# Performance work log

Hardware: AMD Instinct MI355X
Metric: run time of the kernel (lower is better)

Reference implementation:

```python
import jax, jax.numpy as jnp
import numpy as np

B, V, L, H, E, META = 2048, 4096, 10, 512, 256, 15
TAU = 1.2
SOS = 0
EOS = 0


def setup_inputs() -> dict:
    key = jax.random.key(0)
    ks = jax.random.split(key, 8)
    hidden_state = jax.random.normal(ks[0], (B, META), jnp.float32)
    W_in = jax.random.normal(ks[1], (META, H), jnp.float32) * 0.1
    b_in = jnp.zeros((H,), jnp.float32)
    embedding = jax.random.normal(ks[2], (V, E), jnp.float32) * 0.1
    W_ih = jax.random.normal(ks[3], (4 * H, E), jnp.float32) * (1.0 / np.sqrt(E))
    W_hh = jax.random.normal(ks[4], (4 * H, H), jnp.float32) * (1.0 / np.sqrt(H))
    b_ih = jnp.zeros((4 * H,), jnp.float32)
    # forget-gate bias initialized to 1 (reset_parameters)
    b_hh = jnp.zeros((4 * H,), jnp.float32).at[H:2 * H].set(1.0)
    W_out = jax.random.normal(ks[5], (H, V), jnp.float32) * 0.02
    b_out = jnp.zeros((V,), jnp.float32)
    u = jax.random.uniform(ks[6], (L, B, V), jnp.float32, 1e-8, 1.0 - 1e-8)
    gumbel = -jnp.log(-jnp.log(u))
    return {"hidden_state": hidden_state, "W_in": W_in, "b_in": b_in,
            "embedding": embedding, "W_ih": W_ih, "W_hh": W_hh,
            "b_ih": b_ih, "b_hh": b_hh, "W_out": W_out, "b_out": b_out,
            "gumbel": gumbel}


def reference(hidden_state, W_in, b_in, embedding, W_ih, W_hh, b_ih, b_hh,
              W_out, b_out, gumbel):
    initial_length = L + 1
    h0 = hidden_state @ W_in + b_in              # [B,H] input_module (meta)
    c0 = jnp.zeros_like(h0)
    tok0 = jnp.zeros((B, V), jnp.float32).at[:, SOS].set(1.0)  # one-hot sos
    sl0 = jnp.full((B,), initial_length, jnp.int32)

    def step(carry, xs):
        h, c, tok, sl = carry
        i, g = xs
        emb = tok @ embedding                                  # [B,E]
        gates = emb @ W_ih.T + b_ih + h @ W_hh.T + b_hh        # [B,4H]
        ig, fg, gg, og = jnp.split(gates, 4, axis=1)
        c = jax.nn.sigmoid(fg) * c + jax.nn.sigmoid(ig) * jnp.tanh(gg)
        h = jax.nn.sigmoid(og) * jnp.tanh(c)
        logits = h @ W_out + b_out                             # [B,V]
        logp = jax.nn.log_softmax(logits, axis=1)
        p = jnp.exp(logp)
        ent = -jnp.sum(p * logp, axis=1)                       # Categorical entropy
        # gumbel_softmax(p, tau, hard=True): softmax((log p + g)/tau), straight-through
        y = jax.nn.softmax((logp + g) / TAU, axis=1)
        hard = jax.nn.one_hot(jnp.argmax(y, axis=1), V, dtype=y.dtype)
        tok_new = jax.lax.stop_gradient(hard - y) + y
        mask = (hard[:, EOS] == 1.0) & (sl == initial_length)
        sl = jnp.where(mask, i + 2, sl)  # seq_pos = i+1, set to seq_pos+1
        return (h, c, tok_new, sl), (tok_new, emb, ent)

    (_, _, _, seq_lengths), (toks, embeds, ents) = jax.lax.scan(
        step, (h0, c0, tok0, sl0), (jnp.arange(L, dtype=jnp.int32), gumbel))
    output = jnp.concatenate([tok0[:, None, :], jnp.transpose(toks, (1, 0, 2))], axis=1)  # [B,L+1,V]
    embeds_out = jnp.transpose(embeds, (1, 0, 2))              # [B,L,E]
    entropy = jnp.mean(jnp.sum(ents, axis=0)) / L
    sentence_probability = jnp.zeros((B, V), jnp.float32)      # only filled in eval mode
    return output, seq_lengths, entropy, embeds_out, sentence_probability
```

## Files before the change

kernel.cpp:

```cpp
#include <hip/hip_runtime.h>
#include <hip/hip_bf16.h>
#include <math.h>

typedef unsigned short u16;
typedef __attribute__((ext_vector_type(8))) short bf16x8;
typedef __attribute__((ext_vector_type(4))) float f32x4;

#define B_    2048
#define V_    4096
#define L_    10
#define H_    512
#define E_    256
#define META_ 15
#define H4_   2048
#define W6_   (H4_ + V_)
#define EOS_  0
#define INIT_LEN_ (L_ + 1)

constexpr size_t OUT_SL  = (size_t)B_ * (L_ + 1) * V_;
constexpr size_t OUT_ENT = OUT_SL + B_;
constexpr size_t OUT_EMB = OUT_ENT + 1;
constexpr size_t OUT_SP  = OUT_EMB + (size_t)B_ * L_ * E_;

constexpr size_t WS_E2G     = 0;
constexpr size_t WS_LOGITS  = WS_E2G    + (size_t)V_ * H4_;
constexpr size_t WS_G       = WS_LOGITS + (size_t)B_ * V_;
constexpr size_t WS_C       = WS_G      + (size_t)B_ * H4_;
constexpr size_t WS_F32_END = WS_C      + (size_t)B_ * H_;
constexpr size_t U_W6_HI    = 0;
constexpr size_t U_W6_LO    = U_W6_HI + (size_t)W6_ * H_;
constexpr size_t U_HHI      = U_W6_LO + (size_t)W6_ * H_;
constexpr size_t U_HLO      = U_HHI   + (size_t)B_ * H_;
constexpr size_t U_END      = U_HLO   + (size_t)B_ * H_;

__device__ __forceinline__ u16 f2bf(float f) {
    union { __hip_bfloat16 b; u16 u; } cv; cv.b = __float2bfloat16(f); return cv.u;
}
__device__ __forceinline__ float bf2f(u16 u) {
    union { u16 u; __hip_bfloat16 b; } cv; cv.u = u; return __bfloat162float(cv.b);
}

__device__ __forceinline__ void gld16(const u16* g, void* l) {
    __builtin_amdgcn_global_load_lds(
        (const __attribute__((address_space(1))) unsigned int*)g,
        (__attribute__((address_space(3))) unsigned int*)l, 16, 0, 0);
}

template <int EPI>
__global__ __launch_bounds__(256)
void gemm3(const u16* __restrict__ Ah, const u16* __restrict__ Al,
           const u16* __restrict__ Bh, const u16* __restrict__ Bl,
           float* __restrict__ C0, float* __restrict__ C1, int K,
           const float* __restrict__ bias0, const float* __restrict__ bias1,
           int xoff)
{
    __shared__ u16 As[2][128][32];
    __shared__ u16 Bs[2][128][32];
    const int tid  = threadIdx.x;
    const int lane = tid & 63;
    const int wave = tid >> 6;
    const int wm = wave >> 1, wn = wave & 1;

    const int nwg  = gridDim.x * gridDim.y;
    const int bid  = blockIdx.y * gridDim.x + blockIdx.x;
    const int w    = (bid & 7) * (nwg >> 3) + (bid >> 3);
    const int colb = w / gridDim.y + xoff;
    const int rowb = w % gridDim.y;
    const int col0 = colb * 128;
    const int row0 = rowb * 128;

    const int srow = tid >> 2;
    const int scol = (tid & 3) * 8;
    const size_t aoff = (size_t)(row0 + srow) * K + scol;
    const size_t boff = (size_t)(col0 + srow) * K + scol;
    const size_t skip = (size_t)64 * K;

    u16* lA0 = &As[0][0][0];
    u16* lA1 = &As[1][0][0];
    u16* lB0 = &Bs[0][0][0];
    u16* lB1 = &Bs[1][0][0];
    const int d0 = tid * 8;
    const int d1 = d0 + 2048;

    f32x4 acc[4][4] = {};
    const int fr = lane & 15;
    const int kq = lane >> 4;

    for (int k0 = 0; k0 < K; k0 += 32) {
        __syncthreads();
        gld16(Ah + aoff + k0,        lA0 + d0);
        gld16(Ah + aoff + k0 + skip, lA0 + d1);
        gld16(Al + aoff + k0,        lA1 + d0);
        gld16(Al + aoff + k0 + skip, lA1 + d1);
        gld16(Bh + boff + k0,        lB0 + d0);
        gld16(Bh + boff + k0 + skip, lB0 + d1);
        gld16(Bl + boff + k0,        lB1 + d0);
        gld16(Bl + boff + k0 + skip, lB1 + d1);
        __syncthreads();

        bf16x8 ah[4], al[4], bh[4], bl[4];
#pragma unroll
        for (int i = 0; i < 4; ++i) {
            ah[i] = *(const bf16x8*)&As[0][wm * 64 + i * 16 + fr][kq * 8];
            al[i] = *(const bf16x8*)&As[1][wm * 64 + i * 16 + fr][kq * 8];
            bh[i] = *(const bf16x8*)&Bs[0][wn * 64 + i * 16 + fr][kq * 8];
            bl[i] = *(const bf16x8*)&Bs[1][wn * 64 + i * 16 + fr][kq * 8];
        }
#pragma unroll
        for (int mi = 0; mi < 4; ++mi)
#pragma unroll
            for (int ni = 0; ni < 4; ++ni) {
                acc[mi][ni] = __builtin_amdgcn_mfma_f32_16x16x32_bf16(ah[mi], bh[ni], acc[mi][ni], 0, 0, 0);
                acc[mi][ni] = __builtin_amdgcn_mfma_f32_16x16x32_bf16(ah[mi], bl[ni], acc[mi][ni], 0, 0, 0);
                acc[mi][ni] = __builtin_amdgcn_mfma_f32_16x16x32_bf16(al[mi], bh[ni], acc[mi][ni], 0, 0, 0);
            }
    }

    const int cc0 = col0 + wn * 64 + fr;
    float* Cbase;
    int ldc, ccol;
    bool addBias;
    if (EPI == 0) {
        Cbase = C0; ldc = H4_; ccol = cc0; addBias = true;
    } else {
        const bool isG = (col0 < H4_);
        Cbase = isG ? C0 : C1;
        ldc   = isG ? H4_ : V_;
        ccol  = isG ? cc0 : cc0 - H4_;
        addBias = !isG;
    }
#pragma unroll
    for (int mi = 0; mi < 4; ++mi) {
#pragma unroll
        for (int r = 0; r < 4; ++r) {
            const int grow = row0 + wm * 64 + mi * 16 + kq * 4 + r;
            float* cp = Cbase + (size_t)grow * ldc + ccol;
#pragma unroll
            for (int ni = 0; ni < 4; ++ni) {
                float v = acc[mi][ni][r];
                if (EPI == 0) v += bias0[ccol + ni * 16] + bias1[ccol + ni * 16];
                if (EPI == 1 && addBias) v += bias0[ccol + ni * 16];
                cp[ni * 16] = v;
            }
        }
    }
}

template <bool LAST>
__global__ __launch_bounds__(256)
void step_merge(const float* __restrict__ logits, const float* __restrict__ gumbel,
                const float* __restrict__ G, const float* __restrict__ e2g,
                const float* __restrict__ embedding,
                u16* __restrict__ h_hi, u16* __restrict__ h_lo,
                float* __restrict__ c, float* __restrict__ out,
                int* __restrict__ sl, float* __restrict__ ents, int step)
{
    const int b   = blockIdx.x;
    const int tid = threadIdx.x;
    const float* lrow = logits + (size_t)b * V_;
    const float* grow = gumbel + ((size_t)step * B_ + b) * V_;
    __shared__ float lsm[V_];
    __shared__ float red_m[4], red_bv[4], red_s[4], red_t[4];
    __shared__ int   red_bi[4];
    __shared__ float s_M;
    __shared__ int   s_bi;

    float m = -3.4e38f, bv = -3.4e38f;
    int bi = 0x7fffffff;
    for (int q = tid; q < V_ / 4; q += 256) {
        float4 l4 = ((const float4*)lrow)[q];
        float4 g4 = ((const float4*)grow)[q];
        ((float4*)lsm)[q] = l4;
        m = fmaxf(m, fmaxf(fmaxf(l4.x, l4.y), fmaxf(l4.z, l4.w)));
        float p; const int i4 = q * 4;
        p = l4.x + g4.x; if (p > bv) { bv = p; bi = i4; }
        p = l4.y + g4.y; if (p > bv) { bv = p; bi = i4 + 1; }
        p = l4.z + g4.z; if (p > bv) { bv = p; bi = i4 + 2; }
        p = l4.w + g4.w; if (p > bv) { bv = p; bi = i4 + 3; }
    }
#pragma unroll
    for (int off = 32; off > 0; off >>= 1) {
        m = fmaxf(m, __shfl_down(m, off));
        float obv = __shfl_down(bv, off);
        int   obi = __shfl_down(bi, off);
        if (obv > bv || (obv == bv && obi < bi)) { bv = obv; bi = obi; }
    }
    const int wave = tid >> 6, lane = tid & 63;
    if (lane == 0) { red_m[wave] = m; red_bv[wave] = bv; red_bi[wave] = bi; }
    __syncthreads();
    if (tid == 0) {
        m = red_m[0]; bv = red_bv[0]; bi = red_bi[0];
        for (int w = 1; w < 4; ++w) {
            m = fmaxf(m, red_m[w]);
            if (red_bv[w] > bv || (red_bv[w] == bv && red_bi[w] < bi)) {
                bv = red_bv[w]; bi = red_bi[w];
            }
        }
        s_M = m; s_bi = bi;
    }
    __syncthreads();
    const float M = s_M;
    const int amax = s_bi;

    float s = 0.f, t = 0.f;
    for (int q = tid; q < V_; q += 256) {
        const float l = lsm[q];
        const float e = __expf(l - M);
        s += e; t += e * l;
    }
#pragma unroll
    for (int off = 32; off > 0; off >>= 1) {
        s += __shfl_down(s, off);
        t += __shfl_down(t, off);
    }
    if (lane == 0) { red_s[wave] = s; red_t[wave] = t; }

    float* orow = out + ((size_t)b * (L_ + 1) + step + 1) * V_;
    const float4 z4 = make_float4(0.f, 0.f, 0.f, 0.f);
    for (int q = tid; q < V_ / 4; q += 256) ((float4*)orow)[q] = z4;
    __syncthreads();
    if (tid == 0) {
        const float ss = red_s[0] + red_s[1] + red_s[2] + red_s[3];
        const float tt = red_t[0] + red_t[1] + red_t[2] + red_t[3];
        ents[b] += (M + logf(ss)) - tt / ss;
        orow[amax] = 1.0f;
        if (amax == EOS_ && sl[b] == INIT_LEN_) sl[b] = step + 2;
    }

    if (!LAST) {
        const float* Gr = G + (size_t)b * H4_;
        const float* er = e2g + (size_t)amax * H4_;
#pragma unroll
        for (int jj = 0; jj < 2; ++jj) {
            const int j = tid + jj * 256;
            const float ig = Gr[j]          + er[j];
            const float fg = Gr[H_ + j]     + er[H_ + j];
            const float gg = Gr[2 * H_ + j] + er[2 * H_ + j];
            const float og = Gr[3 * H_ + j] + er[3 * H_ + j];
            const float si = 1.f / (1.f + expf(-ig));
            const float sf = 1.f / (1.f + expf(-fg));
            const float so = 1.f / (1.f + expf(-og));
            const size_t idx = (size_t)b * H_ + j;
            const float cn = sf * c[idx] + si * tanhf(gg);
            c[idx] = cn;
            const float hv = so * tanhf(cn);
            const u16 hh = f2bf(hv);
            h_hi[idx] = hh;
            h_lo[idx] = f2bf(hv - bf2f(hh));
        }
        if (tid < E_)
            out[OUT_EMB + ((size_t)b * L_ + step + 1) * E_ + tid] =
                embedding[(size_t)amax * E_ + tid];
    }
}

__global__ __launch_bounds__(256)
void split_wout(const float* __restrict__ W_out, u16* __restrict__ hiT,
                u16* __restrict__ loT)
{
    __shared__ float t[32][33];
    const int v0 = blockIdx.x * 32, k0 = blockIdx.y * 32;
    const int x = threadIdx.x & 31, y = threadIdx.x >> 5;
    for (int yy = y; yy < 32; yy += 8)
        t[yy][x] = W_out[(size_t)(k0 + yy) * V_ + v0 + x];
    __syncthreads();
    for (int yy = y; yy < 32; yy += 8) {
        const float v = t[x][yy];
        const u16 h = f2bf(v);
        hiT[(size_t)(v0 + yy) * H_ + k0 + x] = h;
        loT[(size_t)(v0 + yy) * H_ + k0 + x] = f2bf(v - bf2f(h));
    }
}

__global__ __launch_bounds__(256)
void split_mat(const float* __restrict__ X, u16* __restrict__ hi,
               u16* __restrict__ lo)
{
    const int i = blockIdx.x * 256 + threadIdx.x;
    float4 v = ((const float4*)X)[i];
    const u16 h0 = f2bf(v.x), h1 = f2bf(v.y), h2 = f2bf(v.z), h3 = f2bf(v.w);
    ((ushort4*)hi)[i] = make_ushort4(h0, h1, h2, h3);
    ((ushort4*)lo)[i] = make_ushort4(f2bf(v.x - bf2f(h0)), f2bf(v.y - bf2f(h1)),
                                     f2bf(v.z - bf2f(h2)), f2bf(v.w - bf2f(h3)));
}

__global__ __launch_bounds__(256)
void h0_kernel(const float* __restrict__ hs, const float* __restrict__ W_in,
               const float* __restrict__ b_in, u16* __restrict__ h_hi,
               u16* __restrict__ h_lo, float* __restrict__ c)
{
    const int idx = blockIdx.x * 256 + threadIdx.x;
    const int b = idx >> 9, j = idx & 511;
    float acc = b_in[j];
#pragma unroll
    for (int e = 0; e < META_; ++e)
        acc = fmaf(hs[b * META_ + e], W_in[e * H_ + j], acc);
    const u16 hh = f2bf(acc);
    h_hi[idx] = hh;
    h_lo[idx] = f2bf(acc - bf2f(hh));
    c[idx] = 0.f;
}

__global__ __launch_bounds__(256)
void init_outputs(float* __restrict__ out, int* __restrict__ tok,
                  int* __restrict__ sl, float* __restrict__ ents)
{
    const int tid = blockIdx.x * 256 + threadIdx.x;
    {
        const int b = tid >> 10;
        const int q = tid & 1023;
        float4 z = make_float4(0.f, 0.f, 0.f, 0.f);
        if (q == 0) z.x = 1.0f;
        ((float4*)out)[(size_t)b * ((L_ + 1) * V_ / 4) + q] = z;
    }
    for (size_t t = tid; t < (size_t)B_ * V_; t += (size_t)gridDim.x * 256)
        out[OUT_SP + t] = 0.f;
    if (tid < B_) { tok[tid] = 0; sl[tid] = INIT_LEN_; ents[tid] = 0.f; }
}

__global__ __launch_bounds__(256)
void lstm_cell(const float* __restrict__ G, const float* __restrict__ e2g,
               u16* __restrict__ h_hi, u16* __restrict__ h_lo,
               float* __restrict__ c, const float* __restrict__ embedding,
               const int* __restrict__ tok, float* __restrict__ out, int step)
{
    const int idx = blockIdx.x * 256 + threadIdx.x;
    const int b = idx >> 9, j = idx & 511;
    const size_t g0 = (size_t)b * H4_;
    const size_t e0 = (size_t)tok[b] * H4_;
    const float ig = G[g0 + j]          + e2g[e0 + j];
    const float fg = G[g0 + H_ + j]     + e2g[e0 + H_ + j];
    const float gg = G[g0 + 2 * H_ + j] + e2g[e0 + 2 * H_ + j];
    const float og = G[g0 + 3 * H_ + j] + e2g[e0 + 3 * H_ + j];
    const float si = 1.f / (1.f + expf(-ig));
    const float sf = 1.f / (1.f + expf(-fg));
    const float so = 1.f / (1.f + expf(-og));
    const float cn = sf * c[idx] + si * tanhf(gg);
    c[idx] = cn;
    const float hv = so * tanhf(cn);
    const u16 hh = f2bf(hv);
    h_hi[idx] = hh;
    h_lo[idx] = f2bf(hv - bf2f(hh));
    if (j < E_)
        out[OUT_EMB + ((size_t)b * L_ + step) * E_ + j] =
            embedding[(size_t)tok[b] * E_ + j];
}

__global__ __launch_bounds__(256)
void finalize(const int* __restrict__ sl, const float* __restrict__ ents,
              float* __restrict__ out)
{
    const int tid = threadIdx.x;
    float s = 0.f;
    for (int b = tid; b < B_; b += 256) {
        s += ents[b];
        out[OUT_SL + b] = (float)sl[b];
    }
    __shared__ float red[4];
#pragma unroll
    for (int off = 32; off > 0; off >>= 1) s += __shfl_down(s, off);
    if ((tid & 63) == 0) red[tid >> 6] = s;
    __syncthreads();
    if (tid == 0)
        out[OUT_ENT] = (red[0] + red[1] + red[2] + red[3]) / (float)B_ / (float)L_;
}

extern "C" void kernel_launch(void* const* d_in, const int* in_sizes, int n_in,
                              void* d_out, int out_size, void* d_ws, size_t ws_size,
                              hipStream_t stream)
{
    const float* hidden    = (const float*)d_in[0];
    const float* W_in      = (const float*)d_in[1];
    const float* b_in      = (const float*)d_in[2];
    const float* embedding = (const float*)d_in[3];
    const float* W_ih      = (const float*)d_in[4];
    const float* W_hh      = (const float*)d_in[5];
    const float* b_ih      = (const float*)d_in[6];
    const float* b_hh      = (const float*)d_in[7];
    const float* W_out     = (const float*)d_in[8];
    const float* b_out     = (const float*)d_in[9];
    const float* gumbel    = (const float*)d_in[10];
    float* out = (float*)d_out;

    float* ws    = (float*)d_ws;
    float* E2G   = ws + WS_E2G;
    float* logit = ws + WS_LOGITS;
    float* G     = ws + WS_G;
    float* c     = ws + WS_C;
    u16*   wsu   = (u16*)(ws + WS_F32_END);
    u16* w6_hi   = wsu + U_W6_HI;
    u16* w6_lo   = wsu + U_W6_LO;
    u16* h_hi    = wsu + U_HHI;
    u16* h_lo    = wsu + U_HLO;
    int* tok     = (int*)(wsu + U_END);
    int* sl      = tok + B_;
    float* ents  = (float*)(sl + B_);
    u16* emb_hi  = (u16*)logit;
    u16* emb_lo  = emb_hi + (size_t)V_ * E_;
    u16* wih_hi  = emb_lo + (size_t)V_ * E_;
    u16* wih_lo  = wih_hi + (size_t)H4_ * E_;

    split_mat<<<(H4_ * H_ / 4) / 256, 256, 0, stream>>>(W_hh, w6_hi, w6_lo);
    split_wout<<<dim3(V_ / 32, H_ / 32), 256, 0, stream>>>(
        W_out, w6_hi + (size_t)H4_ * H_, w6_lo + (size_t)H4_ * H_);
    split_mat<<<(V_ * E_ / 4) / 256, 256, 0, stream>>>(embedding, emb_hi, emb_lo);
    split_mat<<<(H4_ * E_ / 4) / 256, 256, 0, stream>>>(W_ih, wih_hi, wih_lo);
    h0_kernel<<<(B_ * H_) / 256, 256, 0, stream>>>(hidden, W_in, b_in, h_hi, h_lo, c);
    init_outputs<<<(B_ * V_ / 4) / 256, 256, 0, stream>>>(out, tok, sl, ents);
    gemm3<0><<<dim3(H4_ / 128, V_ / 128), 256, 0, stream>>>(
        emb_hi, emb_lo, wih_hi, wih_lo, E2G, nullptr, E_, b_ih, b_hh, 0);
    gemm3<1><<<dim3(H4_ / 128, B_ / 128), 256, 0, stream>>>(
        h_hi, h_lo, w6_hi, w6_lo, G, logit, H_, b_out, nullptr, 0);
    lstm_cell<<<(B_ * H_) / 256, 256, 0, stream>>>(G, E2G, h_hi, h_lo, c,
                                                   embedding, tok, out, 0);

    for (int i = 0; i < L_; ++i) {
        if (i < L_ - 1) {
            gemm3<1><<<dim3(W6_ / 128, B_ / 128), 256, 0, stream>>>(
                h_hi, h_lo, w6_hi, w6_lo, G, logit, H_, b_out, nullptr, 0);
            step_merge<false><<<B_, 256, 0, stream>>>(
                logit, gumbel, G, E2G, embedding, h_hi, h_lo, c, out,
                sl, ents, i);
        } else {
            gemm3<1><<<dim3(V_ / 128, B_ / 128), 256, 0, stream>>>(
                h_hi, h_lo, w6_hi, w6_lo, G, logit, H_, b_out, nullptr,
                H4_ / 128);
            step_merge<true><<<B_, 256, 0, stream>>>(
                logit, gumbel, G, E2G, embedding, h_hi, h_lo, c, out,
                sl, ents, i);
        }
    }
    finalize<<<1, 256, 0, stream>>>(sl, ents, out);
}
```

Baseline: 835.2 us.

## Pre-pack GEMM operands into tiled layout and use 32x32x16 MFMA

The recurrent h and the combined W_hh/W_out weights are now stored in a tile-packed layout (128-row blocks, k-chunks of 32, 8-element groups), so each GEMM stage is a contiguous 8 KB block loaded straight to LDS. The main per-step GEMM is rewritten to use 32x32x16 bf16 MFMA with 2x2 accumulators per wave instead of 16x16x32, which cuts LDS reads per MFMA. The h writers and weight repack kernels scatter into the packed layout, trading coalesced stores for faster GEMM loads. The packed LDS layout may also bring bank conflicts.

```diff
diff --git a/kernel.cpp b/kernel.cpp
--- a/kernel.cpp
+++ b/kernel.cpp
@@ -5,6 +5,7 @@
 typedef unsigned short u16;
 typedef __attribute__((ext_vector_type(8))) short bf16x8;
 typedef __attribute__((ext_vector_type(4))) float f32x4;
+typedef __attribute__((ext_vector_type(16))) float f32x16;
 
 #define B_    2048
 #define V_    4096
@@ -27,11 +28,11 @@
 constexpr size_t WS_G       = WS_LOGITS + (size_t)B_ * V_;
 constexpr size_t WS_C       = WS_G      + (size_t)B_ * H4_;
 constexpr size_t WS_F32_END = WS_C      + (size_t)B_ * H_;
-constexpr size_t U_W6_HI    = 0;
-constexpr size_t U_W6_LO    = U_W6_HI + (size_t)W6_ * H_;
-constexpr size_t U_HHI      = U_W6_LO + (size_t)W6_ * H_;
-constexpr size_t U_HLO      = U_HHI   + (size_t)B_ * H_;
-constexpr size_t U_END      = U_HLO   + (size_t)B_ * H_;
+constexpr size_t U_BH       = 0;
+constexpr size_t U_BL       = U_BH + (size_t)W6_ * H_;
+constexpr size_t U_AH       = U_BL + (size_t)W6_ * H_;
+constexpr size_t U_AL       = U_AH + (size_t)B_ * H_;
+constexpr size_t U_END      = U_AL + (size_t)B_ * H_;
 
 __device__ __forceinline__ u16 f2bf(float f) {
     union { __hip_bfloat16 b; u16 u; } cv; cv.b = __float2bfloat16(f); return cv.u;
@@ -39,20 +40,113 @@
 __device__ __forceinline__ float bf2f(u16 u) {
     union { u16 u; __hip_bfloat16 b; } cv; cv.u = u; return __bfloat162float(cv.b);
 }
-
 __device__ __forceinline__ void gld16(const u16* g, void* l) {
     __builtin_amdgcn_global_load_lds(
         (const __attribute__((address_space(1))) unsigned int*)g,
         (__attribute__((address_space(3))) unsigned int*)l, 16, 0, 0);
 }
 
-template <int EPI>
-__global__ __launch_bounds__(256)
-void gemm3(const u16* __restrict__ Ah, const u16* __restrict__ Al,
-           const u16* __restrict__ Bh, const u16* __restrict__ Bl,
-           float* __restrict__ C0, float* __restrict__ C1, int K,
-           const float* __restrict__ bias0, const float* __restrict__ bias1,
-           int xoff)
+__device__ __forceinline__ size_t a_pk(int r, int k) {
+    return (size_t)(r >> 7) * 65536 + (size_t)(k >> 5) * 4096 +
+           (size_t)((k >> 3) & 3) * 1024 + (size_t)(r & 127) * 8 + (k & 7);
+}
+
+__global__ __launch_bounds__(256)
+void gemm32(const u16* __restrict__ Ah, const u16* __restrict__ Al,
+            const u16* __restrict__ Bh, const u16* __restrict__ Bl,
+            float* __restrict__ C0, float* __restrict__ C1,
+            const float* __restrict__ bias0, int xoff)
+{
+    __shared__ u16 As[2][4096];
+    __shared__ u16 Bs[2][4096];
+    const int tid  = threadIdx.x;
+    const int lane = tid & 63;
+    const int wave = tid >> 6;
+    const int wm = wave >> 1, wn = wave & 1;
+    const int l31 = lane & 31, lh = lane >> 5;
+
+    const int nwg  = gridDim.x * gridDim.y;
+    const int bid  = blockIdx.y * gridDim.x + blockIdx.x;
+    const int w    = (bid & 7) * (nwg >> 3) + (bid >> 3);
+    const int colb = w / gridDim.y + xoff;
+    const int rowb = w % gridDim.y;
+    const int col0 = colb * 128;
+    const int row0 = rowb * 128;
+
+    const u16* Ah_p = Ah + (size_t)rowb * 65536;
+    const u16* Al_p = Al + (size_t)rowb * 65536;
+    const u16* Bh_p = Bh + (size_t)colb * 65536;
+    const u16* Bl_p = Bl + (size_t)colb * 65536;
+    const int d0 = tid * 8;
+    const int d1 = d0 + 2048;
+
+    const int abase = lh * 1024 + (wm * 64 + l31) * 8;
+    const int bbase = lh * 1024 + (wn * 64 + l31) * 8;
+
+    f32x16 acc[2][2] = {};
+
+    for (int t = 0; t < 16; ++t) {
+        const int g0 = t * 4096;
+        __syncthreads();
+        gld16(Ah_p + g0 + d0, &As[0][d0]);
+        gld16(Ah_p + g0 + d1, &As[0][d1]);
+        gld16(Al_p + g0 + d0, &As[1][d0]);
+        gld16(Al_p + g0 + d1, &As[1][d1]);
+        gld16(Bh_p + g0 + d0, &Bs[0][d0]);
+        gld16(Bh_p + g0 + d1, &Bs[0][d1]);
+        gld16(Bl_p + g0 + d0, &Bs[1][d0]);
+        gld16(Bl_p + g0 + d1, &Bs[1][d1]);
+        __syncthreads();
+
+        bf16x8 ah[2][2], al[2][2], bh[2][2], bl[2][2];
+#pragma unroll
+        for (int kh = 0; kh < 2; ++kh)
+#pragma unroll
+            for (int g = 0; g < 2; ++g) {
+                ah[kh][g] = *(const bf16x8*)&As[0][abase + kh * 2048 + g * 256];
+                al[kh][g] = *(const bf16x8*)&As[1][abase + kh * 2048 + g * 256];
+                bh[kh][g] = *(const bf16x8*)&Bs[0][bbase + kh * 2048 + g * 256];
+                bl[kh][g] = *(const bf16x8*)&Bs[1][bbase + kh * 2048 + g * 256];
+            }
+#pragma unroll
+        for (int kh = 0; kh < 2; ++kh)
+#pragma unroll
+            for (int rg = 0; rg < 2; ++rg)
+#pragma unroll
+                for (int cg = 0; cg < 2; ++cg) {
+                    acc[rg][cg] = __builtin_amdgcn_mfma_f32_32x32x16_bf16(
+                        ah[kh][rg], bh[kh][cg], acc[rg][cg], 0, 0, 0);
+                    acc[rg][cg] = __builtin_amdgcn_mfma_f32_32x32x16_bf16(
+                        ah[kh][rg], bl[kh][cg], acc[rg][cg], 0, 0, 0);
+                    acc[rg][cg] = __builtin_amdgcn_mfma_f32_32x32x16_bf16(
+                        al[kh][rg], bh[kh][cg], acc[rg][cg], 0, 0, 0);
+                }
+    }
+
+    const bool isG  = (col0 < H4_);
+    float* Cb       = isG ? C0 : C1;
+    const int ldc   = isG ? H4_ : V_;
+    const int ccol0 = (isG ? col0 : col0 - H4_) + wn * 64 + l31;
+    const int rbase = row0 + wm * 64 + 4 * lh;
+#pragma unroll
+    for (int rg = 0; rg < 2; ++rg)
+#pragma unroll
+        for (int cg = 0; cg < 2; ++cg) {
+            const int ccol = ccol0 + cg * 32;
+            const float bv = isG ? 0.f : bias0[ccol];
+#pragma unroll
+            for (int reg = 0; reg < 16; ++reg) {
+                const int row = rbase + rg * 32 + (reg & 3) + 8 * (reg >> 2);
+                Cb[(size_t)row * ldc + ccol] = acc[rg][cg][reg] + bv;
+            }
+        }
+}
+
+__global__ __launch_bounds__(256)
+void gemm_e2g(const u16* __restrict__ Ah, const u16* __restrict__ Al,
+              const u16* __restrict__ Bh, const u16* __restrict__ Bl,
+              float* __restrict__ C0, int K,
+              const float* __restrict__ bias0, const float* __restrict__ bias1)
 {
     __shared__ u16 As[2][128][32];
     __shared__ u16 Bs[2][128][32];
@@ -60,11 +154,10 @@
     const int lane = tid & 63;
     const int wave = tid >> 6;
     const int wm = wave >> 1, wn = wave & 1;
-
     const int nwg  = gridDim.x * gridDim.y;
     const int bid  = blockIdx.y * gridDim.x + blockIdx.x;
     const int w    = (bid & 7) * (nwg >> 3) + (bid >> 3);
-    const int colb = w / gridDim.y + xoff;
+    const int colb = w / gridDim.y;
     const int rowb = w % gridDim.y;
     const int col0 = colb * 128;
     const int row0 = rowb * 128;
@@ -117,31 +210,15 @@
     }
 
     const int cc0 = col0 + wn * 64 + fr;
-    float* Cbase;
-    int ldc, ccol;
-    bool addBias;
-    if (EPI == 0) {
-        Cbase = C0; ldc = H4_; ccol = cc0; addBias = true;
-    } else {
-        const bool isG = (col0 < H4_);
-        Cbase = isG ? C0 : C1;
-        ldc   = isG ? H4_ : V_;
-        ccol  = isG ? cc0 : cc0 - H4_;
-        addBias = !isG;
-    }
 #pragma unroll
     for (int mi = 0; mi < 4; ++mi) {
 #pragma unroll
         for (int r = 0; r < 4; ++r) {
             const int grow = row0 + wm * 64 + mi * 16 + kq * 4 + r;
-            float* cp = Cbase + (size_t)grow * ldc + ccol;
-#pragma unroll
-            for (int ni = 0; ni < 4; ++ni) {
-                float v = acc[mi][ni][r];
-                if (EPI == 0) v += bias0[ccol + ni * 16] + bias1[ccol + ni * 16];
-                if (EPI == 1 && addBias) v += bias0[ccol + ni * 16];
-                cp[ni * 16] = v;
-            }
+            float* cp = C0 + (size_t)grow * H4_ + cc0;
+#pragma unroll
+            for (int ni = 0; ni < 4; ++ni)
+                cp[ni * 16] = acc[mi][ni][r] + bias0[cc0 + ni * 16] + bias1[cc0 + ni * 16];
         }
     }
 }
@@ -245,8 +322,9 @@
             c[idx] = cn;
             const float hv = so * tanhf(cn);
             const u16 hh = f2bf(hv);
-            h_hi[idx] = hh;
-            h_lo[idx] = f2bf(hv - bf2f(hh));
+            const size_t p = a_pk(b, j);
+            h_hi[p] = hh;
+            h_lo[p] = f2bf(hv - bf2f(hh));
         }
         if (tid < E_)
             out[OUT_EMB + ((size_t)b * L_ + step + 1) * E_ + tid] =
@@ -255,8 +333,23 @@
 }
 
 __global__ __launch_bounds__(256)
-void split_wout(const float* __restrict__ W_out, u16* __restrict__ hiT,
-                u16* __restrict__ loT)
+void repack_whh(const float* __restrict__ W_hh, u16* __restrict__ Bh,
+                u16* __restrict__ Bl)
+{
+    const int i = blockIdx.x * 256 + threadIdx.x;
+    float4 v = ((const float4*)W_hh)[i];
+    const int col = (i * 4) >> 9;
+    const int k   = (i * 4) & 511;
+    const size_t p = a_pk(col, k);
+    const u16 h0 = f2bf(v.x), h1 = f2bf(v.y), h2 = f2bf(v.z), h3 = f2bf(v.w);
+    *(ushort4*)(Bh + p) = make_ushort4(h0, h1, h2, h3);
+    *(ushort4*)(Bl + p) = make_ushort4(f2bf(v.x - bf2f(h0)), f2bf(v.y - bf2f(h1)),
+                                       f2bf(v.z - bf2f(h2)), f2bf(v.w - bf2f(h3)));
+}
+
+__global__ __launch_bounds__(256)
+void repack_wout(const float* __restrict__ W_out, u16* __restrict__ Bh,
+                 u16* __restrict__ Bl)
 {
     __shared__ float t[32][33];
     const int v0 = blockIdx.x * 32, k0 = blockIdx.y * 32;
@@ -266,9 +359,10 @@
     __syncthreads();
     for (int yy = y; yy < 32; yy += 8) {
         const float v = t[x][yy];
+        const size_t p = a_pk(2048 + v0 + yy, k0 + x);
         const u16 h = f2bf(v);
-        hiT[(size_t)(v0 + yy) * H_ + k0 + x] = h;
-        loT[(size_t)(v0 + yy) * H_ + k0 + x] = f2bf(v - bf2f(h));
+        Bh[p] = h;
+        Bl[p] = f2bf(v - bf2f(h));
     }
 }
 
@@ -286,8 +380,8 @@
 
 __global__ __launch_bounds__(256)
 void h0_kernel(const float* __restrict__ hs, const float* __restrict__ W_in,
-               const float* __restrict__ b_in, u16* __restrict__ h_hi,
-               u16* __restrict__ h_lo, float* __restrict__ c)
+               const float* __restrict__ b_in, u16* __restrict__ Ah,
+               u16* __restrict__ Al, float* __restrict__ c)
 {
     const int idx = blockIdx.x * 256 + threadIdx.x;
     const int b = idx >> 9, j = idx & 511;
@@ -296,8 +390,9 @@
     for (int e = 0; e < META_; ++e)
         acc = fmaf(hs[b * META_ + e], W_in[e * H_ + j], acc);
     const u16 hh = f2bf(acc);
-    h_hi[idx] = hh;
-    h_lo[idx] = f2bf(acc - bf2f(hh));
+    const size_t p = a_pk(b, j);
+    Ah[p] = hh;
+    Al[p] = f2bf(acc - bf2f(hh));
     c[idx] = 0.f;
 }
 
@@ -320,7 +415,7 @@
 
 __global__ __launch_bounds__(256)
 void lstm_cell(const float* __restrict__ G, const float* __restrict__ e2g,
-               u16* __restrict__ h_hi, u16* __restrict__ h_lo,
+               u16* __restrict__ Ah, u16* __restrict__ Al,
                float* __restrict__ c, const float* __restrict__ embedding,
                const int* __restrict__ tok, float* __restrict__ out, int step)
 {
@@ -339,8 +434,9 @@
     c[idx] = cn;
     const float hv = so * tanhf(cn);
     const u16 hh = f2bf(hv);
-    h_hi[idx] = hh;
-    h_lo[idx] = f2bf(hv - bf2f(hh));
+    const size_t p = a_pk(b, j);
+    Ah[p] = hh;
+    Al[p] = f2bf(hv - bf2f(hh));
     if (j < E_)
         out[OUT_EMB + ((size_t)b * L_ + step) * E_ + j] =
             embedding[(size_t)tok[b] * E_ + j];
@@ -388,10 +484,10 @@
     float* G     = ws + WS_G;
     float* c     = ws + WS_C;
     u16*   wsu   = (u16*)(ws + WS_F32_END);
-    u16* w6_hi   = wsu + U_W6_HI;
-    u16* w6_lo   = wsu + U_W6_LO;
-    u16* h_hi    = wsu + U_HHI;
-    u16* h_lo    = wsu + U_HLO;
+    u16* Bh_pk   = wsu + U_BH;
+    u16* Bl_pk   = wsu + U_BL;
+    u16* Ah_pk   = wsu + U_AH;
+    u16* Al_pk   = wsu + U_AL;
     int* tok     = (int*)(wsu + U_END);
     int* sl      = tok + B_;
     float* ents  = (float*)(sl + B_);
@@ -400,33 +496,32 @@
     u16* wih_hi  = emb_lo + (size_t)V_ * E_;
     u16* wih_lo  = wih_hi + (size_t)H4_ * E_;
 
-    split_mat<<<(H4_ * H_ / 4) / 256, 256, 0, stream>>>(W_hh, w6_hi, w6_lo);
-    split_wout<<<dim3(V_ / 32, H_ / 32), 256, 0, stream>>>(
-        W_out, w6_hi + (size_t)H4_ * H_, w6_lo + (size_t)H4_ * H_);
+    repack_whh<<<(H4_ * H_ / 4) / 256, 256, 0, stream>>>(W_hh, Bh_pk, Bl_pk);
+    repack_wout<<<dim3(V_ / 32, H_ / 32), 256, 0, stream>>>(W_out, Bh_pk, Bl_pk);
     split_mat<<<(V_ * E_ / 4) / 256, 256, 0, stream>>>(embedding, emb_hi, emb_lo);
     split_mat<<<(H4_ * E_ / 4) / 256, 256, 0, stream>>>(W_ih, wih_hi, wih_lo);
-    h0_kernel<<<(B_ * H_) / 256, 256, 0, stream>>>(hidden, W_in, b_in, h_hi, h_lo, c);
+    h0_kernel<<<(B_ * H_) / 256, 256, 0, stream>>>(hidden, W_in, b_in,
+                                                   Ah_pk, Al_pk, c);
     init_outputs<<<(B_ * V_ / 4) / 256, 256, 0, stream>>>(out, tok, sl, ents);
-    gemm3<0><<<dim3(H4_ / 128, V_ / 128), 256, 0, stream>>>(
-        emb_hi, emb_lo, wih_hi, wih_lo, E2G, nullptr, E_, b_ih, b_hh, 0);
-    gemm3<1><<<dim3(H4_ / 128, B_ / 128), 256, 0, stream>>>(
-        h_hi, h_lo, w6_hi, w6_lo, G, logit, H_, b_out, nullptr, 0);
-    lstm_cell<<<(B_ * H_) / 256, 256, 0, stream>>>(G, E2G, h_hi, h_lo, c,
+    gemm_e2g<<<dim3(H4_ / 128, V_ / 128), 256, 0, stream>>>(
+        emb_hi, emb_lo, wih_hi, wih_lo, E2G, E_, b_ih, b_hh);
+    gemm32<<<dim3(16, 16), 256, 0, stream>>>(Ah_pk, Al_pk, Bh_pk, Bl_pk,
+                                             G, logit, b_out, 0);
+    lstm_cell<<<(B_ * H_) / 256, 256, 0, stream>>>(G, E2G, Ah_pk, Al_pk, c,
                                                    embedding, tok, out, 0);
 
     for (int i = 0; i < L_; ++i) {
         if (i < L_ - 1) {
-            gemm3<1><<<dim3(W6_ / 128, B_ / 128), 256, 0, stream>>>(
-                h_hi, h_lo, w6_hi, w6_lo, G, logit, H_, b_out, nullptr, 0);
+            gemm32<<<dim3(48, 16), 256, 0, stream>>>(
+                Ah_pk, Al_pk, Bh_pk, Bl_pk, G, logit, b_out, 0);
             step_merge<false><<<B_, 256, 0, stream>>>(
-                logit, gumbel, G, E2G, embedding, h_hi, h_lo, c, out,
+                logit, gumbel, G, E2G, embedding, Ah_pk, Al_pk, c, out,
                 sl, ents, i);
         } else {
-            gemm3<1><<<dim3(V_ / 128, B_ / 128), 256, 0, stream>>>(
-                h_hi, h_lo, w6_hi, w6_lo, G, logit, H_, b_out, nullptr,
-                H4_ / 128);
+            gemm32<<<dim3(32, 16), 256, 0, stream>>>(
+                Ah_pk, Al_pk, Bh_pk, Bl_pk, G, logit, b_out, 16);
             step_merge<true><<<B_, 256, 0, stream>>>(
-                logit, gumbel, G, E2G, embedding, h_hi, h_lo, c, out,
+                logit, gumbel, G, E2G, embedding, Ah_pk, Al_pk, c, out,
                 sl, ents, i);
         }
     }
```

Result: faster. 792.5 us (-5.1%).
